# Kernel tuning notes

Hardware: AMD Instinct MI355X
Metric: run time of the kernel (lower is better)

## Reference

```python
import jax, jax.numpy as jnp
import numpy as np

SIZE = 512
LANG_NUM = 8
B, S, D = 32, 2048, SIZE


def setup_inputs() -> dict:
    key = jax.random.key(0)
    ks = jax.random.split(key, 10)
    sc = 1.0 / np.sqrt(D)
    inp = {
        "old_x": jax.random.normal(ks[0], (B, S, D), jnp.float32),
        "x": jax.random.normal(ks[1], (B, S, D), jnp.float32),
        "lang": jax.random.randint(ks[2], (B,), 0, LANG_NUM, jnp.int32),
        # shared linear (no bias): y = x @ W.T
        "share_W": jax.random.uniform(ks[3], (D, D), jnp.float32, -sc, sc),
        # per-language expert linears (no bias)
        "langs_W": jax.random.uniform(ks[4], (LANG_NUM, D, D), jnp.float32, -sc, sc),
        # per-language gate: layer1 (D->D with bias), layer2 (D->1 with bias)
        "gate_W1": jax.random.uniform(ks[5], (LANG_NUM, D, D), jnp.float32, -sc, sc),
        "gate_b1": jax.random.uniform(ks[6], (LANG_NUM, D), jnp.float32, -sc, sc),
        "gate_W2": jax.random.uniform(ks[7], (LANG_NUM, D), jnp.float32, -sc, sc),
        "gate_b2": jax.random.uniform(ks[8], (LANG_NUM,), jnp.float32, -sc, sc),
    }
    return inp


def reference(old_x, x, lang, share_W, langs_W, gate_W1, gate_b1, gate_W2, gate_b2):
    # shared path: [B,S,D] @ [D,D].T
    share_h = jnp.einsum("bsd,ed->bse", x, share_W)
    # gather per-sample expert weights by lang index
    Wl = langs_W[lang]            # [B,D,D]
    W1 = gate_W1[lang]            # [B,D,D]
    b1 = gate_b1[lang]            # [B,D]
    W2 = gate_W2[lang]            # [B,D]
    b2 = gate_b2[lang]            # [B]
    langs_h = jnp.einsum("bsd,bed->bse", x, Wl)
    # GateLayer on old_x: relu(L1(x)) + x -> L2 -> sigmoid
    h = jax.nn.relu(jnp.einsum("bsd,bed->bse", old_x, W1) + b1[:, None, :]) + old_x
    gate_logit = jnp.einsum("bsd,bd->bs", h, W2) + b2[:, None]
    gate_prob = jax.nn.sigmoid(gate_logit)[:, :, None]   # [B,S,1]
    return share_h * (1.0 - gate_prob) + langs_h * gate_prob
```

## Files before the change

### kernel.cpp

```cpp
#include <hip/hip_runtime.h>
#include <hip/hip_bf16.h>

#define B_ 32
#define S_ 2048
#define D_ 512

typedef __attribute__((ext_vector_type(8))) short bf16x8;
typedef __attribute__((ext_vector_type(4))) float f32x4;
typedef unsigned short ushort_t;

__device__ __forceinline__ float b2f(ushort_t u) {
  union { unsigned int i; float f; } v; v.i = ((unsigned int)u) << 16; return v.f;
}
__device__ __forceinline__ ushort_t f2b(float f) {
  union { float f; unsigned int i; } v; v.f = f;
  return (ushort_t)((v.i + 0x7FFFu + ((v.i >> 16) & 1u)) >> 16);
}

__device__ __forceinline__ f32x4 mfma16(bf16x8 a, bf16x8 b, f32x4 c) {
  return __builtin_amdgcn_mfma_f32_16x16x32_bf16(a, b, c, 0, 0, 0);
}

__global__ void detect_kernel(const unsigned int* __restrict__ w, int* __restrict__ flag) {
  __shared__ int cnt;
  if (threadIdx.x == 0) cnt = 0;
  __syncthreads();
  int c = 0;
  #pragma unroll
  for (int i = 0; i < 4; ++i) {
    unsigned int v = w[threadIdx.x + i * 256];
    unsigned int e = (v >> 7) & 0xFFu;
    if (e >= 110u && e <= 140u) ++c;
  }
  atomicAdd(&cnt, c);
  __syncthreads();
  if (threadIdx.x == 0) flag[0] = (cnt > 512) ? 1 : 0;
}

template <int DT>
__device__ __forceinline__ float ldf(const void* p, size_t idx) {
  if constexpr (DT == 0) return ((const float*)p)[idx];
  else                   return b2f(((const ushort_t*)p)[idx]);
}

__device__ __forceinline__ bf16x8 read_frag(const ushort_t* tile, int row, int quad) {
  int g = quad ^ ((row >> 1) & 3);
  return *(const bf16x8*)(tile + row * 32 + g * 8);
}


template <int DT> struct TR16 { float4 f[4]; bf16x8 h[2]; };

template <int DT>
__device__ __forceinline__ void t16_load(const void* gv, size_t base, int tid, TR16<DT>& t) {
  const int row = tid >> 1, half = tid & 1;
  const size_t off = base + (size_t)row * D_ + half * 16;
  if constexpr (DT == 0) {
    const float4* s = (const float4*)((const float*)gv + off);
    t.f[0] = s[0]; t.f[1] = s[1]; t.f[2] = s[2]; t.f[3] = s[3];
  } else {
    const bf16x8* s = (const bf16x8*)((const ushort_t*)gv + off);
    t.h[0] = s[0]; t.h[1] = s[1];
  }
}
template <int DT>
__device__ __forceinline__ void t16_store(ushort_t* tile, int tid, const TR16<DT>& t) {
  const int row = tid >> 1, half = tid & 1;
  bf16x8 ch0, ch1;
  if constexpr (DT == 0) {
    ushort_t u[16];
    u[0]  = f2b(t.f[0].x); u[1]  = f2b(t.f[0].y); u[2]  = f2b(t.f[0].z); u[3]  = f2b(t.f[0].w);
    u[4]  = f2b(t.f[1].x); u[5]  = f2b(t.f[1].y); u[6]  = f2b(t.f[1].z); u[7]  = f2b(t.f[1].w);
    u[8]  = f2b(t.f[2].x); u[9]  = f2b(t.f[2].y); u[10] = f2b(t.f[2].z); u[11] = f2b(t.f[2].w);
    u[12] = f2b(t.f[3].x); u[13] = f2b(t.f[3].y); u[14] = f2b(t.f[3].z); u[15] = f2b(t.f[3].w);
    ch0 = *(const bf16x8*)u; ch1 = *(const bf16x8*)(u + 8);
  } else { ch0 = t.h[0]; ch1 = t.h[1]; }
  const int swz = (row >> 1) & 3, c0 = half * 2;
  *(bf16x8*)(tile + row * 32 + (((c0    ) ^ swz) << 3)) = ch0;
  *(bf16x8*)(tile + row * 32 + (((c0 + 1) ^ swz) << 3)) = ch1;
}

template <int DT> struct TRA { float4 f[2]; bf16x8 h; };

template <int DT>
__device__ __forceinline__ void ta_load(const void* gv, size_t base, int tid, TRA<DT>& t) {
  const int row = tid >> 2, g = tid & 3;
  const size_t off = base + (size_t)row * D_ + g * 8;
  if constexpr (DT == 0) {
    const float4* s = (const float4*)((const float*)gv + off);
    t.f[0] = s[0]; t.f[1] = s[1];
  } else {
    t.h = *(const bf16x8*)((const ushort_t*)gv + off);
  }
}
template <int DT>
__device__ __forceinline__ void ta_store(ushort_t* tile, int tid, const TRA<DT>& t) {
  const int row = tid >> 2, g = tid & 3;
  bf16x8 ch;
  if constexpr (DT == 0) {
    ushort_t u[8];
    u[0] = f2b(t.f[0].x); u[1] = f2b(t.f[0].y); u[2] = f2b(t.f[0].z); u[3] = f2b(t.f[0].w);
    u[4] = f2b(t.f[1].x); u[5] = f2b(t.f[1].y); u[6] = f2b(t.f[1].z); u[7] = f2b(t.f[1].w);
    ch = *(const bf16x8*)u;
  } else ch = t.h;
  const int swz = (row >> 1) & 3;
  *(bf16x8*)(tile + row * 32 + ((g ^ swz) << 3)) = ch;
}

template <int DT> struct TRB { float4 f[8]; bf16x8 h[4]; };

template <int DT>
__device__ __forceinline__ void tb_load(const void* gv, size_t base, int tid, TRB<DT>& t) {
  const size_t off = base + (size_t)tid * D_;
  if constexpr (DT == 0) {
    const float4* s = (const float4*)((const float*)gv + off);
    #pragma unroll
    for (int i = 0; i < 8; ++i) t.f[i] = s[i];
  } else {
    const bf16x8* s = (const bf16x8*)((const ushort_t*)gv + off);
    #pragma unroll
    for (int i = 0; i < 4; ++i) t.h[i] = s[i];
  }
}
template <int DT>
__device__ __forceinline__ void tb_store(ushort_t* tile, int tid, const TRB<DT>& t) {
  const int row = tid, swz = (row >> 1) & 3;
  #pragma unroll
  for (int g = 0; g < 4; ++g) {
    bf16x8 ch;
    if constexpr (DT == 0) {
      ushort_t u[8];
      float4 a = t.f[2 * g], b = t.f[2 * g + 1];
      u[0] = f2b(a.x); u[1] = f2b(a.y); u[2] = f2b(a.z); u[3] = f2b(a.w);
      u[4] = f2b(b.x); u[5] = f2b(b.y); u[6] = f2b(b.z); u[7] = f2b(b.w);
      ch = *(const bf16x8*)u;
    } else ch = t.h[g];
    *(bf16x8*)(tile + row * 32 + ((g ^ swz) << 3)) = ch;
  }
}

struct GateSmem {
  alignas(16) ushort_t As[2][128 * 32];
  alignas(16) ushort_t Bs[2][512 * 32];
  float b1s[512], w2s[512], logit[128];
};
struct OutSmem {
  alignas(16) ushort_t As[2][128 * 32];
  alignas(16) ushort_t Ss[2][128 * 32];
  alignas(16) ushort_t Ls[2][128 * 32];
};

template <int DT>
__device__ __forceinline__ void gate_body(const void* __restrict__ old_x,
    const int* __restrict__ lang, const void* __restrict__ W1,
    const void* __restrict__ b1, const void* __restrict__ W2,
    const void* __restrict__ b2p, float* __restrict__ gate, GateSmem& sm) {
  int bid = blockIdx.y * gridDim.x + blockIdx.x;
  int swz = (bid & 7) * 64 + (bid >> 3);
  const int s0 = (swz & 15) * 128;
  const int b  = swz >> 4;
  const int tid  = threadIdx.x;
  const int wave = tid >> 6, lane = tid & 63, quad = lane >> 4, ln = lane & 15;
  const int m_off = (wave >> 2) * 64;
  const int n_off = (wave & 3) * 128;
  const int lg = lang[b];

  sm.b1s[tid] = ldf<DT>(b1, (size_t)lg * 512 + tid);
  sm.w2s[tid] = ldf<DT>(W2, (size_t)lg * 512 + tid);
  if (tid < 128) sm.logit[tid] = 0.f;

  const size_t Aoff = ((size_t)b * S_ + s0) * D_;
  const size_t Boff = (size_t)lg * D_ * D_;

  f32x4 acc[4][8];
  #pragma unroll
  for (int i = 0; i < 4; ++i)
    #pragma unroll
    for (int j = 0; j < 8; ++j) { f32x4 z = {0.f, 0.f, 0.f, 0.f}; acc[i][j] = z; }

  TRA<DT> ta; TRB<DT> tb;
  tb_load<DT>(W1, Boff, tid, tb);
  ta_load<DT>(old_x, Aoff, tid, ta);
  tb_store<DT>(sm.Bs[0], tid, tb);
  ta_store<DT>(sm.As[0], tid, ta);
  __syncthreads();

  const int rrow  = tid >> 2, rg = tid & 3;
  const int rslot = (rg ^ ((rrow >> 1) & 3)) << 3;
  float res = 0.f;

  for (int step = 0; step < 16; ++step) {
    const int cur = step & 1;
    if (step < 15) {
      tb_load<DT>(W1, Boff + (step + 1) * 32, tid, tb);
      ta_load<DT>(old_x, Aoff + (step + 1) * 32, tid, ta);
    }
    bf16x8 af[4];
    #pragma unroll
    for (int mf = 0; mf < 4; ++mf)
      af[mf] = read_frag(sm.As[cur], m_off + mf * 16 + ln, quad);
    {
      bf16x8 rv = *(const bf16x8*)(sm.As[cur] + rrow * 32 + rslot);
      #pragma unroll
      for (int j = 0; j < 8; ++j)
        res += b2f((ushort_t)rv[j]) * sm.w2s[step * 32 + rg * 8 + j];
    }
    #pragma unroll
    for (int nh = 0; nh < 2; ++nh) {
      bf16x8 bfr[4];
      #pragma unroll
      for (int nf = 0; nf < 4; ++nf)
        bfr[nf] = read_frag(sm.Bs[cur], n_off + (nh * 4 + nf) * 16 + ln, quad);
      #pragma unroll
      for (int mf = 0; mf < 4; ++mf)
        #pragma unroll
        for (int nf = 0; nf < 4; ++nf)
          acc[mf][nh * 4 + nf] = mfma16(af[mf], bfr[nf], acc[mf][nh * 4 + nf]);
    }
    if (step < 15) {
      const int nxt = cur ^ 1;
      tb_store<DT>(sm.Bs[nxt], tid, tb);
      ta_store<DT>(sm.As[nxt], tid, ta);
    }
    __syncthreads();
  }
  atomicAdd(&sm.logit[rrow], res);

  float logacc[16];
  #pragma unroll
  for (int i = 0; i < 16; ++i) logacc[i] = 0.f;
  #pragma unroll
  for (int nf = 0; nf < 8; ++nf) {
    int e = n_off + nf * 16 + ln;
    float b1v = sm.b1s[e], w2v = sm.w2s[e];
    #pragma unroll
    for (int mf = 0; mf < 4; ++mf)
      #pragma unroll
      for (int r = 0; r < 4; ++r) {
        float v = acc[mf][nf][r] + b1v;
        logacc[mf * 4 + r] += fmaxf(v, 0.f) * w2v;
      }
  }
  #pragma unroll
  for (int off = 1; off < 16; off <<= 1)
    #pragma unroll
    for (int i = 0; i < 16; ++i)
      logacc[i] += __shfl_xor(logacc[i], off, 64);
  if (ln == 0) {
    #pragma unroll
    for (int mf = 0; mf < 4; ++mf)
      #pragma unroll
      for (int r = 0; r < 4; ++r)
        atomicAdd(&sm.logit[m_off + mf * 16 + quad * 4 + r], logacc[mf * 4 + r]);
  }
  __syncthreads();
  if (tid < 128) {
    float bb = ldf<DT>(b2p, lg);
    float l = sm.logit[tid] + bb;
    gate[(size_t)b * S_ + s0 + tid] = 1.f / (1.f + expf(-l));
  }
}

__global__ __launch_bounds__(512, 2)
void gate_kernel(const void* __restrict__ old_x, const int* __restrict__ lang,
                 const void* __restrict__ W1, const void* __restrict__ b1,
                 const void* __restrict__ W2, const void* __restrict__ b2,
                 const int* __restrict__ flag, float* __restrict__ gate) {
  __shared__ GateSmem sm;
  if (flag[0] == 0) gate_body<0>(old_x, lang, W1, b1, W2, b2, gate, sm);
  else              gate_body<1>(old_x, lang, W1, b1, W2, b2, gate, sm);
}

template <int DT>
__device__ __forceinline__ void out_body(const void* __restrict__ x,
    const int* __restrict__ lang, const void* __restrict__ shareW,
    const void* __restrict__ langsW, const float* __restrict__ gate,
    void* __restrict__ out, OutSmem& sm) {
  int bid = (blockIdx.z * gridDim.y + blockIdx.y) * gridDim.x + blockIdx.x;
  int swz = (bid & 7) * 256 + (bid >> 3);
  const int e0 = (swz & 3) * 128;
  const int s0 = ((swz >> 2) & 15) * 128;
  const int b  = swz >> 6;
  const int tid  = threadIdx.x;
  const int wave = tid >> 6, lane = tid & 63, quad = lane >> 4, ln = lane & 15;
  const int m_off = (wave >> 1) * 64, n_off = (wave & 1) * 64;
  const int lg = lang[b];

  const size_t Aoff = ((size_t)b * S_ + s0) * D_;
  const size_t Soff = (size_t)e0 * D_;
  const size_t Loff = ((size_t)lg * D_ + e0) * D_;

  f32x4 accS[4][4], accL[4][4];
  #pragma unroll
  for (int i = 0; i < 4; ++i)
    #pragma unroll
    for (int j = 0; j < 4; ++j) {
      f32x4 z = {0.f, 0.f, 0.f, 0.f};
      accS[i][j] = z; accL[i][j] = z;
    }

  TR16<DT> ta, ts, tl;
  t16_load<DT>(shareW, Soff, tid, ts);
  t16_load<DT>(langsW, Loff, tid, tl);
  t16_load<DT>(x,      Aoff, tid, ta);
  t16_store<DT>(sm.Ss[0], tid, ts);
  t16_store<DT>(sm.Ls[0], tid, tl);
  t16_store<DT>(sm.As[0], tid, ta);
  __syncthreads();

  for (int step = 0; step < 16; ++step) {
    const int cur = step & 1;
    if (step < 15) {
      t16_load<DT>(shareW, Soff + (step + 1) * 32, tid, ts);
      t16_load<DT>(langsW, Loff + (step + 1) * 32, tid, tl);
      t16_load<DT>(x,      Aoff + (step + 1) * 32, tid, ta);
    }
    bf16x8 af[4], sf[4], lf[4];
    #pragma unroll
    for (int mf = 0; mf < 4; ++mf)
      af[mf] = read_frag(sm.As[cur], m_off + mf * 16 + ln, quad);
    #pragma unroll
    for (int nf = 0; nf < 4; ++nf) {
      sf[nf] = read_frag(sm.Ss[cur], n_off + nf * 16 + ln, quad);
      lf[nf] = read_frag(sm.Ls[cur], n_off + nf * 16 + ln, quad);
    }
    #pragma unroll
    for (int mf = 0; mf < 4; ++mf)
      #pragma unroll
      for (int nf = 0; nf < 4; ++nf) {
        accS[mf][nf] = mfma16(af[mf], sf[nf], accS[mf][nf]);
        accL[mf][nf] = mfma16(af[mf], lf[nf], accL[mf][nf]);
      }
    if (step < 15) {
      const int nxt = cur ^ 1;
      t16_store<DT>(sm.Ss[nxt], tid, ts);
      t16_store<DT>(sm.Ls[nxt], tid, tl);
      t16_store<DT>(sm.As[nxt], tid, ta);
    }
    __syncthreads();
  }

  #pragma unroll
  for (int mf = 0; mf < 4; ++mf) {
    int srow = s0 + m_off + mf * 16 + quad * 4;
    float gv[4];
    #pragma unroll
    for (int r = 0; r < 4; ++r) gv[r] = gate[(size_t)b * S_ + srow + r];
    #pragma unroll
    for (int nf = 0; nf < 4; ++nf) {
      int col = e0 + n_off + nf * 16 + ln;
      f32x4 cs = accS[mf][nf], cl = accL[mf][nf];
      #pragma unroll
      for (int r = 0; r < 4; ++r) {
        float v = cs[r] + gv[r] * (cl[r] - cs[r]);
        size_t idx = ((size_t)b * S_ + srow + r) * D_ + col;
        if constexpr (DT == 0)
          __builtin_nontemporal_store(v, (float*)out + idx);
        else
          __builtin_nontemporal_store(f2b(v), (ushort_t*)out + idx);
      }
    }
  }
}

__global__ __launch_bounds__(256, 2)
void out_kernel(const void* __restrict__ x, const int* __restrict__ lang,
                const void* __restrict__ shareW, const void* __restrict__ langsW,
                const float* __restrict__ gate, const int* __restrict__ flag,
                void* __restrict__ out) {
  __shared__ OutSmem sm;
  if (flag[0] == 0) out_body<0>(x, lang, shareW, langsW, gate, out, sm);
  else              out_body<1>(x, lang, shareW, langsW, gate, out, sm);
}

extern "C" void kernel_launch(void* const* d_in, const int* in_sizes, int n_in,
                              void* d_out, int out_size, void* d_ws, size_t ws_size,
                              hipStream_t stream) {
  const void* old_x  = d_in[0];
  const void* x      = d_in[1];
  const int*  lang   = (const int*)d_in[2];
  const void* shareW = d_in[3];
  const void* langsW = d_in[4];
  const void* gW1    = d_in[5];
  const void* gb1    = d_in[6];
  const void* gW2    = d_in[7];
  const void* gb2    = d_in[8];

  float* gate = (float*)d_ws;
  int*   flag = (int*)((char*)d_ws + (size_t)B_ * S_ * sizeof(float));

  detect_kernel<<<1, 256, 0, stream>>>((const unsigned int*)old_x, flag);

  dim3 g1(S_ / 128, B_);
  gate_kernel<<<g1, dim3(512), 0, stream>>>(old_x, lang, gW1, gb1, gW2, gb2, flag, gate);

  dim3 g2(D_ / 128, S_ / 128, B_);
  out_kernel<<<g2, dim3(256), 0, stream>>>(x, lang, shareW, langsW, gate, flag, d_out);
}
```

Baseline: 550.4 us.

## Pre-convert weights to swizzled bf16 tiles and stage them via direct global-to-LDS loads

Adds a convert kernel that converts all weight matrices to bf16 once per call. It writes them into the workspace already laid out as swizzled 128x32 tiles, and converts the bias and gate vectors to fp32. The gate and output GEMM kernels then stage weight tiles with global_load_lds straight into shared memory. This removes per-block fp32 loads, the bf16 conversion and the register round-trip for the weight operand. It also drops the nontemporal output stores. In exchange there is an extra launch and extra workspace traffic for the converted weights.

```diff
diff --git a/kernel.cpp b/kernel.cpp
--- a/kernel.cpp
+++ b/kernel.cpp
@@ -5,6 +5,15 @@
 #define S_ 2048
 #define D_ 512
 
+#define WS_GATE  0
+#define WS_FLAG  262144
+#define WS_SW    266240
+#define WS_LW    (WS_SW + 64 * 8192)
+#define WS_W1    (WS_LW + 512 * 8192)
+#define WS_B1F   (WS_W1 + 512 * 8192)
+#define WS_W2F   (WS_B1F + 16384)
+#define WS_B2F   (WS_W2F + 16384)
+
 typedef __attribute__((ext_vector_type(8))) short bf16x8;
 typedef __attribute__((ext_vector_type(4))) float f32x4;
 typedef unsigned short ushort_t;
@@ -19,6 +28,12 @@
 
 __device__ __forceinline__ f32x4 mfma16(bf16x8 a, bf16x8 b, f32x4 c) {
   return __builtin_amdgcn_mfma_f32_16x16x32_bf16(a, b, c, 0, 0, 0);
+}
+
+__device__ __forceinline__ void gload16(const void* g, void* l) {
+  __builtin_amdgcn_global_load_lds(
+      (const __attribute__((address_space(1))) unsigned int*)g,
+      (__attribute__((address_space(3))) unsigned int*)l, 16, 0, 0);
 }
 
 __global__ void detect_kernel(const unsigned int* __restrict__ w, int* __restrict__ flag) {
@@ -37,17 +52,10 @@
   if (threadIdx.x == 0) flag[0] = (cnt > 512) ? 1 : 0;
 }
 
-template <int DT>
-__device__ __forceinline__ float ldf(const void* p, size_t idx) {
-  if constexpr (DT == 0) return ((const float*)p)[idx];
-  else                   return b2f(((const ushort_t*)p)[idx]);
-}
-
 __device__ __forceinline__ bf16x8 read_frag(const ushort_t* tile, int row, int quad) {
   int g = quad ^ ((row >> 1) & 3);
   return *(const bf16x8*)(tile + row * 32 + g * 8);
 }
-
 
 template <int DT> struct TR16 { float4 f[4]; bf16x8 h[2]; };
 
@@ -107,35 +115,39 @@
   *(bf16x8*)(tile + row * 32 + ((g ^ swz) << 3)) = ch;
 }
 
-template <int DT> struct TRB { float4 f[8]; bf16x8 h[4]; };
-
-template <int DT>
-__device__ __forceinline__ void tb_load(const void* gv, size_t base, int tid, TRB<DT>& t) {
-  const size_t off = base + (size_t)tid * D_;
-  if constexpr (DT == 0) {
-    const float4* s = (const float4*)((const float*)gv + off);
-    #pragma unroll
-    for (int i = 0; i < 8; ++i) t.f[i] = s[i];
+__global__ __launch_bounds__(256)
+void convert_kernel(const void* __restrict__ shareW, const void* __restrict__ langsW,
+                    const void* __restrict__ gW1, const void* __restrict__ gb1,
+                    const void* __restrict__ gW2, const void* __restrict__ gb2,
+                    const int* __restrict__ flag, char* __restrict__ ws) {
+  const int t = blockIdx.x, tid = threadIdx.x;
+  const int dt = flag[0];
+  if (t < 1088) {
+    const void* src; ushort_t* dst; size_t sb;
+    if (t < 64) {
+      src = shareW; dst = (ushort_t*)(ws + WS_SW) + (size_t)t * 4096;
+      sb = ((size_t)(t >> 4) * 128) * D_ + (size_t)(t & 15) * 32;
+    } else if (t < 576) {
+      const int t2 = t - 64;
+      src = langsW; dst = (ushort_t*)(ws + WS_LW) + (size_t)t2 * 4096;
+      sb = ((size_t)(t2 >> 6) * 512 + (size_t)((t2 >> 4) & 3) * 128) * D_ + (size_t)(t2 & 15) * 32;
+    } else {
+      const int t3 = t - 576;
+      src = gW1; dst = (ushort_t*)(ws + WS_W1) + (size_t)t3 * 4096;
+      sb = ((size_t)(t3 >> 6) * 512 + (size_t)((t3 >> 4) & 3) * 128) * D_ + (size_t)(t3 & 15) * 32;
+    }
+    if (dt == 0) { TR16<0> r; t16_load<0>(src, sb, tid, r); t16_store<0>(dst, tid, r); }
+    else         { TR16<1> r; t16_load<1>(src, sb, tid, r); t16_store<1>(dst, tid, r); }
   } else {
-    const bf16x8* s = (const bf16x8*)((const ushort_t*)gv + off);
-    #pragma unroll
-    for (int i = 0; i < 4; ++i) t.h[i] = s[i];
-  }
-}
-template <int DT>
-__device__ __forceinline__ void tb_store(ushort_t* tile, int tid, const TRB<DT>& t) {
-  const int row = tid, swz = (row >> 1) & 3;
-  #pragma unroll
-  for (int g = 0; g < 4; ++g) {
-    bf16x8 ch;
-    if constexpr (DT == 0) {
-      ushort_t u[8];
-      float4 a = t.f[2 * g], b = t.f[2 * g + 1];
-      u[0] = f2b(a.x); u[1] = f2b(a.y); u[2] = f2b(a.z); u[3] = f2b(a.w);
-      u[4] = f2b(b.x); u[5] = f2b(b.y); u[6] = f2b(b.z); u[7] = f2b(b.w);
-      ch = *(const bf16x8*)u;
-    } else ch = t.h[g];
-    *(bf16x8*)(tile + row * 32 + ((g ^ swz) << 3)) = ch;
+    float* b1f = (float*)(ws + WS_B1F);
+    float* w2f = (float*)(ws + WS_W2F);
+    float* b2w = (float*)(ws + WS_B2F);
+    for (int i = tid; i < 4096; i += 256) {
+      b1f[i] = dt ? b2f(((const ushort_t*)gb1)[i]) : ((const float*)gb1)[i];
+      w2f[i] = dt ? b2f(((const ushort_t*)gW2)[i]) : ((const float*)gW2)[i];
+    }
+    if (tid < 8)
+      b2w[tid] = dt ? b2f(((const ushort_t*)gb2)[tid]) : ((const float*)gb2)[tid];
   }
 }
 
@@ -152,9 +164,9 @@
 
 template <int DT>
 __device__ __forceinline__ void gate_body(const void* __restrict__ old_x,
-    const int* __restrict__ lang, const void* __restrict__ W1,
-    const void* __restrict__ b1, const void* __restrict__ W2,
-    const void* __restrict__ b2p, float* __restrict__ gate, GateSmem& sm) {
+    const int* __restrict__ lang, const ushort_t* __restrict__ w1t,
+    const float* __restrict__ b1f, const float* __restrict__ w2f,
+    const float* __restrict__ b2w, float* __restrict__ gate, GateSmem& sm) {
   int bid = blockIdx.y * gridDim.x + blockIdx.x;
   int swz = (bid & 7) * 64 + (bid >> 3);
   const int s0 = (swz & 15) * 128;
@@ -165,12 +177,23 @@
   const int n_off = (wave & 3) * 128;
   const int lg = lang[b];
 
-  sm.b1s[tid] = ldf<DT>(b1, (size_t)lg * 512 + tid);
-  sm.w2s[tid] = ldf<DT>(W2, (size_t)lg * 512 + tid);
+  sm.b1s[tid] = b1f[lg * 512 + tid];
+  sm.w2s[tid] = w2f[lg * 512 + tid];
   if (tid < 128) sm.logit[tid] = 0.f;
 
   const size_t Aoff = ((size_t)b * S_ + s0) * D_;
-  const size_t Boff = (size_t)lg * D_ * D_;
+  const ushort_t* w1base = w1t + (size_t)lg * 64 * 4096;
+
+  auto stageB = [&](int kt, int buf) {
+    #pragma unroll
+    for (int c = 0; c < 4; ++c) {
+      const int sl = c * 8 + wave;
+      const int et = sl >> 3;
+      const char* g = (const char*)(w1base + ((size_t)(et * 16 + kt)) * 4096)
+                      + (sl & 7) * 1024 + lane * 16;
+      gload16(g, (char*)sm.Bs[buf] + sl * 1024);
+    }
+  };
 
   f32x4 acc[4][8];
   #pragma unroll
@@ -178,10 +201,9 @@
     #pragma unroll
     for (int j = 0; j < 8; ++j) { f32x4 z = {0.f, 0.f, 0.f, 0.f}; acc[i][j] = z; }
 
-  TRA<DT> ta; TRB<DT> tb;
-  tb_load<DT>(W1, Boff, tid, tb);
+  TRA<DT> ta;
+  stageB(0, 0);
   ta_load<DT>(old_x, Aoff, tid, ta);
-  tb_store<DT>(sm.Bs[0], tid, tb);
   ta_store<DT>(sm.As[0], tid, ta);
   __syncthreads();
 
@@ -192,7 +214,7 @@
   for (int step = 0; step < 16; ++step) {
     const int cur = step & 1;
     if (step < 15) {
-      tb_load<DT>(W1, Boff + (step + 1) * 32, tid, tb);
+      stageB(step + 1, cur ^ 1);
       ta_load<DT>(old_x, Aoff + (step + 1) * 32, tid, ta);
     }
     bf16x8 af[4];
@@ -217,11 +239,7 @@
         for (int nf = 0; nf < 4; ++nf)
           acc[mf][nh * 4 + nf] = mfma16(af[mf], bfr[nf], acc[mf][nh * 4 + nf]);
     }
-    if (step < 15) {
-      const int nxt = cur ^ 1;
-      tb_store<DT>(sm.Bs[nxt], tid, tb);
-      ta_store<DT>(sm.As[nxt], tid, ta);
-    }
+    if (step < 15) ta_store<DT>(sm.As[cur ^ 1], tid, ta);
     __syncthreads();
   }
   atomicAdd(&sm.logit[rrow], res);
@@ -255,30 +273,29 @@
   }
   __syncthreads();
   if (tid < 128) {
-    float bb = ldf<DT>(b2p, lg);
-    float l = sm.logit[tid] + bb;
+    float l = sm.logit[tid] + b2w[lg];
     gate[(size_t)b * S_ + s0 + tid] = 1.f / (1.f + expf(-l));
   }
 }
 
 __global__ __launch_bounds__(512, 2)
 void gate_kernel(const void* __restrict__ old_x, const int* __restrict__ lang,
-                 const void* __restrict__ W1, const void* __restrict__ b1,
-                 const void* __restrict__ W2, const void* __restrict__ b2,
+                 const ushort_t* __restrict__ w1t, const float* __restrict__ b1f,
+                 const float* __restrict__ w2f, const float* __restrict__ b2w,
                  const int* __restrict__ flag, float* __restrict__ gate) {
   __shared__ GateSmem sm;
-  if (flag[0] == 0) gate_body<0>(old_x, lang, W1, b1, W2, b2, gate, sm);
-  else              gate_body<1>(old_x, lang, W1, b1, W2, b2, gate, sm);
+  if (flag[0] == 0) gate_body<0>(old_x, lang, w1t, b1f, w2f, b2w, gate, sm);
+  else              gate_body<1>(old_x, lang, w1t, b1f, w2f, b2w, gate, sm);
 }
 
 template <int DT>
 __device__ __forceinline__ void out_body(const void* __restrict__ x,
-    const int* __restrict__ lang, const void* __restrict__ shareW,
-    const void* __restrict__ langsW, const float* __restrict__ gate,
+    const int* __restrict__ lang, const ushort_t* __restrict__ sWt,
+    const ushort_t* __restrict__ lWt, const float* __restrict__ gate,
     void* __restrict__ out, OutSmem& sm) {
   int bid = (blockIdx.z * gridDim.y + blockIdx.y) * gridDim.x + blockIdx.x;
   int swz = (bid & 7) * 256 + (bid >> 3);
-  const int e0 = (swz & 3) * 128;
+  const int eb = swz & 3, e0 = eb * 128;
   const int s0 = ((swz >> 2) & 15) * 128;
   const int b  = swz >> 6;
   const int tid  = threadIdx.x;
@@ -287,8 +304,20 @@
   const int lg = lang[b];
 
   const size_t Aoff = ((size_t)b * S_ + s0) * D_;
-  const size_t Soff = (size_t)e0 * D_;
-  const size_t Loff = ((size_t)lg * D_ + e0) * D_;
+  const ushort_t* Sbase = sWt + (size_t)eb * 16 * 4096;
+  const ushort_t* Lbase = lWt + ((size_t)(lg * 4 + eb)) * 16 * 4096;
+
+  auto stageSL = [&](int kt, int buf) {
+    #pragma unroll
+    for (int c = 0; c < 2; ++c) {
+      const int sl = c * 4 + wave;
+      const int boff = sl * 1024 + lane * 16;
+      gload16((const char*)(Sbase + (size_t)kt * 4096) + boff,
+              (char*)sm.Ss[buf] + sl * 1024);
+      gload16((const char*)(Lbase + (size_t)kt * 4096) + boff,
+              (char*)sm.Ls[buf] + sl * 1024);
+    }
+  };
 
   f32x4 accS[4][4], accL[4][4];
   #pragma unroll
@@ -299,21 +328,17 @@
       accS[i][j] = z; accL[i][j] = z;
     }
 
-  TR16<DT> ta, ts, tl;
-  t16_load<DT>(shareW, Soff, tid, ts);
-  t16_load<DT>(langsW, Loff, tid, tl);
-  t16_load<DT>(x,      Aoff, tid, ta);
-  t16_store<DT>(sm.Ss[0], tid, ts);
-  t16_store<DT>(sm.Ls[0], tid, tl);
+  TR16<DT> ta;
+  stageSL(0, 0);
+  t16_load<DT>(x, Aoff, tid, ta);
   t16_store<DT>(sm.As[0], tid, ta);
   __syncthreads();
 
   for (int step = 0; step < 16; ++step) {
     const int cur = step & 1;
     if (step < 15) {
-      t16_load<DT>(shareW, Soff + (step + 1) * 32, tid, ts);
-      t16_load<DT>(langsW, Loff + (step + 1) * 32, tid, tl);
-      t16_load<DT>(x,      Aoff + (step + 1) * 32, tid, ta);
+      stageSL(step + 1, cur ^ 1);
+      t16_load<DT>(x, Aoff + (step + 1) * 32, tid, ta);
     }
     bf16x8 af[4], sf[4], lf[4];
     #pragma unroll
@@ -331,12 +356,7 @@
         accS[mf][nf] = mfma16(af[mf], sf[nf], accS[mf][nf]);
         accL[mf][nf] = mfma16(af[mf], lf[nf], accL[mf][nf]);
       }
-    if (step < 15) {
-      const int nxt = cur ^ 1;
-      t16_store<DT>(sm.Ss[nxt], tid, ts);
-      t16_store<DT>(sm.Ls[nxt], tid, tl);
-      t16_store<DT>(sm.As[nxt], tid, ta);
-    }
+    if (step < 15) t16_store<DT>(sm.As[cur ^ 1], tid, ta);
     __syncthreads();
   }
 
@@ -354,10 +374,8 @@
       for (int r = 0; r < 4; ++r) {
         float v = cs[r] + gv[r] * (cl[r] - cs[r]);
         size_t idx = ((size_t)b * S_ + srow + r) * D_ + col;
-        if constexpr (DT == 0)
-          __builtin_nontemporal_store(v, (float*)out + idx);
-        else
-          __builtin_nontemporal_store(f2b(v), (ushort_t*)out + idx);
+        if constexpr (DT == 0) ((float*)out)[idx] = v;
+        else                   ((ushort_t*)out)[idx] = f2b(v);
       }
     }
   }
@@ -365,12 +383,12 @@
 
 __global__ __launch_bounds__(256, 2)
 void out_kernel(const void* __restrict__ x, const int* __restrict__ lang,
-                const void* __restrict__ shareW, const void* __restrict__ langsW,
+                const ushort_t* __restrict__ sWt, const ushort_t* __restrict__ lWt,
                 const float* __restrict__ gate, const int* __restrict__ flag,
                 void* __restrict__ out) {
   __shared__ OutSmem sm;
-  if (flag[0] == 0) out_body<0>(x, lang, shareW, langsW, gate, out, sm);
-  else              out_body<1>(x, lang, shareW, langsW, gate, out, sm);
+  if (flag[0] == 0) out_body<0>(x, lang, sWt, lWt, gate, out, sm);
+  else              out_body<1>(x, lang, sWt, lWt, gate, out, sm);
 }
 
 extern "C" void kernel_launch(void* const* d_in, const int* in_sizes, int n_in,
@@ -386,14 +404,25 @@
   const void* gW2    = d_in[7];
   const void* gb2    = d_in[8];
 
-  float* gate = (float*)d_ws;
-  int*   flag = (int*)((char*)d_ws + (size_t)B_ * S_ * sizeof(float));
+  char*  ws   = (char*)d_ws;
+  float* gate = (float*)(ws + WS_GATE);
+  int*   flag = (int*)(ws + WS_FLAG);
+  const ushort_t* sWt = (const ushort_t*)(ws + WS_SW);
+  const ushort_t* lWt = (const ushort_t*)(ws + WS_LW);
+  const ushort_t* w1t = (const ushort_t*)(ws + WS_W1);
+  const float*    b1f = (const float*)(ws + WS_B1F);
+  const float*    w2f = (const float*)(ws + WS_W2F);
+  const float*    b2w = (const float*)(ws + WS_B2F);
 
   detect_kernel<<<1, 256, 0, stream>>>((const unsigned int*)old_x, flag);
 
+  convert_kernel<<<1089, 256, 0, stream>>>(shareW, langsW, gW1, gb1, gW2, gb2,
+                                           flag, ws);
+
   dim3 g1(S_ / 128, B_);
-  gate_kernel<<<g1, dim3(512), 0, stream>>>(old_x, lang, gW1, gb1, gW2, gb2, flag, gate);
+  gate_kernel<<<g1, dim3(512), 0, stream>>>(old_x, lang, w1t, b1f, w2f, b2w,
+                                            flag, gate);
 
   dim3 g2(D_ / 128, S_ / 128, B_);
-  out_kernel<<<g2, dim3(256), 0, stream>>>(x, lang, shareW, langsW, gate, flag, d_out);
-}
+  out_kernel<<<g2, dim3(256), 0, stream>>>(x, lang, sWt, lWt, gate, flag, d_out);
+}
```

After: 448.4 us. 18.5% less time.
